# Kernel optimization log

Hardware: AMD Instinct MI355X
Metric: run time of the kernel (lower is better)

The kernel has to match this reference:

```python
import jax, jax.numpy as jnp
import numpy as np

B, N, D = 32, 2048, 16
PCD = 2        # point_cloud_dimensions
K_NN = 16      # k nearest neighbours
FILTERS = 64


def setup_inputs() -> dict:
    key = jax.random.key(0)
    k1, k2, k3 = jax.random.split(key, 3)
    x = jax.random.normal(k1, (B, N, D), dtype=jnp.float32)
    # 1x1 Conv2D == dense over the last (channel) dim: W [D, FILTERS], b [FILTERS]
    W = jax.random.normal(k2, (D, FILTERS), dtype=jnp.float32) * (1.0 / np.sqrt(D))
    b = jnp.zeros((FILTERS,), dtype=jnp.float32)
    return {"x": x, "W": W, "b": b}


def reference(x, W, b):
    # points = first PCD channels; features = full input (dynamic_coordinates=True)
    points = x[:, :, :PCD]                                   # [B,N,PCD]
    # squared pairwise distances: ||p_i||^2 + ||p_j||^2 - 2 p_i.p_j  -> [B,N,N]
    sq = jnp.sum(points * points, axis=-1)                   # [B,N]
    dist = sq[:, :, None] + sq[:, None, :] - 2.0 * jnp.einsum(
        'bnd,bmd->bnm', points, points)
    # k nearest neighbours (smallest distance) per point -> [B,N,k]
    _, idx = jax.lax.top_k(-dist, K_NN)
    # gather neighbour features: [B,N,k,D]
    neigh = jax.vmap(lambda f, i: f[i])(x, idx)
    centre = x[:, :, None, :]                                # [B,N,1,D]
    # NOTE: source concatenates along the neighbour axis -> [B,N,k+1,D]
    edges = jnp.concatenate([centre, neigh - centre], axis=2)
    # 1x1 conv (linear activation) over channel dim: [B,N,k+1,FILTERS]
    conv = jnp.einsum('bnkd,df->bnkf', edges, W) + b
    # Max pooling over neighbour axis: [B,N,FILTERS]
    pooled = jnp.max(conv, axis=2)
    # shortcut_input_features=True: concat original features
    return jnp.concatenate([pooled, x], axis=-1)             # [B,N,FILTERS+D]
```

## Files before the change

### kernel.cpp

```cpp
#include <hip/hip_runtime.h>


#define B_  32
#define N_  2048
#define D_  16
#define F_  64
#define K_  16
#define OUTD (F_ + D_)
#define NQ  64
#define NS  4
#define SPLIT (N_ / NS)

__global__ __launch_bounds__(256) void proj_kernel(const float* __restrict__ x,
                                                   const float* __restrict__ W,
                                                   float* __restrict__ Y) {
    __shared__ float Ws[D_ * F_];
    __shared__ float xs[4][D_];
    const int t = threadIdx.x;
    for (int i = t; i < D_ * F_; i += 256) Ws[i] = W[i];
    const int p0 = blockIdx.x * 4;
    if (t < 4 * D_) {
        int pw = t / D_, d = t % D_;
        xs[pw][d] = x[(size_t)(p0 + pw) * D_ + d];
    }
    __syncthreads();
    const int w = t >> 6, f = t & 63;
    float acc = 0.f;
#pragma unroll
    for (int d = 0; d < D_; d++) acc = fmaf(xs[w][d], Ws[d * F_ + f], acc);
    Y[(size_t)(p0 + w) * F_ + f] = acc;
}

__global__ __launch_bounds__(256) void knn_kernel(const float* __restrict__ x,
                                                  int* __restrict__ idx) {
    __shared__ float2 pts[N_];
    __shared__ float  sqs[N_];
    __shared__ float  arr[NS - 1][NQ * 17];
    __shared__ float  Tq[NQ];
    __shared__ int    cnt[NQ];
    __shared__ unsigned short tiebuf[NS][NQ][K_];
    __shared__ int    tiecnt[NS][NQ];

    const int b = blockIdx.x >> 5;
    const int qbase = (blockIdx.x & 31) * NQ;
    const int t = threadIdx.x;
    const int s = t >> 6;
    const int qi = t & 63;
    const int q = qbase + qi;

    const float* xb = x + (size_t)b * N_ * D_;
    for (int m = t; m < N_; m += 256) {
        float2 p = make_float2(xb[m * D_ + 0], xb[m * D_ + 1]);
        pts[m] = p;
        sqs[m] = __fadd_rn(__fmul_rn(p.x, p.x), __fmul_rn(p.y, p.y));
    }
    if (t < NQ) cnt[t] = 0;
    __syncthreads();

    const float2 qp = pts[q];
    const float sqn = sqs[q];

    float key[K_];
#pragma unroll
    for (int j = 0; j < K_; j++) key[j] = INFINITY;

    const int m0 = s * SPLIT, m1 = m0 + SPLIT;
#pragma unroll 2
    for (int m = m0; m < m1; m += 2) {
        float2 pa = pts[m];     float sa = sqs[m];
        float2 pb = pts[m + 1]; float sb = sqs[m + 1];
        float dota = __fmaf_rn(qp.y, pa.y, __fmul_rn(qp.x, pa.x));
        float da   = __fsub_rn(__fadd_rn(sqn, sa), __fmul_rn(2.f, dota));
        float dotb = __fmaf_rn(qp.y, pb.y, __fmul_rn(qp.x, pb.x));
        float db   = __fsub_rn(__fadd_rn(sqn, sb), __fmul_rn(2.f, dotb));
        float y0 = fminf(da, db), y1 = fmaxf(da, db);
#pragma unroll
        for (int j = K_ - 1; j >= 2; j--)
            key[j] = fminf(fminf(key[j], fmaxf(key[j - 1], y0)),
                           fmaxf(key[j - 2], y1));
        key[1] = fminf(fminf(key[1], fmaxf(key[0], y0)), y1);
        key[0] = fminf(key[0], y0);
    }

    if (s > 0) {
#pragma unroll
        for (int j = 0; j < K_; j++) arr[s - 1][qi * 17 + j] = key[j];
    }
    __syncthreads();

    if (s == 0) {
        for (int ss = 0; ss < NS - 1; ss++) {
#pragma unroll
            for (int j = 0; j < K_; j += 2) {
                float y0 = arr[ss][qi * 17 + j];
                float y1 = arr[ss][qi * 17 + j + 1];
#pragma unroll
                for (int jj = K_ - 1; jj >= 2; jj--)
                    key[jj] = fminf(fminf(key[jj], fmaxf(key[jj - 1], y0)),
                                    fmaxf(key[jj - 2], y1));
                key[1] = fminf(fminf(key[1], fmaxf(key[0], y0)), y1);
                key[0] = fminf(key[0], y0);
            }
        }
        Tq[qi] = key[K_ - 1];
    }
    __syncthreads();

    const float T = Tq[qi];
    int* op = idx + ((size_t)b * N_ + q) * K_;
    int tc = 0;
    for (int m = m0; m < m1; m++) {
        float2 p = pts[m];
        float dot = __fmaf_rn(qp.y, p.y, __fmul_rn(qp.x, p.x));
        float d   = __fsub_rn(__fadd_rn(sqn, sqs[m]), __fmul_rn(2.f, dot));
        if (d < T) {
            int slot = atomicAdd(&cnt[qi], 1);
            op[slot] = m;
        } else if (d == T) {
            if (tc < K_) tiebuf[s][qi][tc] = (unsigned short)m;
            tc++;
        }
    }
    tiecnt[s][qi] = (tc < K_) ? tc : K_;
    __syncthreads();

    if (s == 0) {
        int c1 = cnt[qi];
        int w = c1;
        int need = K_ - c1;
        for (int ss = 0; ss < NS && need > 0; ss++) {
            int nn = tiecnt[ss][qi];
            for (int j = 0; j < nn && need > 0; j++) {
                op[w++] = (int)tiebuf[ss][qi][j];
                need--;
            }
        }
    }
}

__global__ __launch_bounds__(256) void pool_kernel(const float* __restrict__ x,
                                                   const float* __restrict__ bias,
                                                   const float* __restrict__ Y,
                                                   const int* __restrict__ idx,
                                                   float* __restrict__ out) {
    const int t = threadIdx.x;
    const int w = t >> 6, f = t & 63;
    const int p = blockIdx.x * 4 + w;
    const int b = p >> 11;
    const size_t pb = (size_t)p;

    const float yn = Y[pb * F_ + f];
    const int* ip = idx + pb * K_;
    float M = -INFINITY;
#pragma unroll
    for (int k = 0; k < K_; k++) {
        int m = ip[k];
        float ym = Y[((size_t)b * N_ + m) * F_ + f];
        M = fmaxf(M, ym);
    }
    float pooled = fmaxf(yn, M - yn) + bias[f];
    out[pb * OUTD + f] = pooled;
    if (f < D_) out[pb * OUTD + F_ + f] = x[pb * D_ + f];
}

extern "C" void kernel_launch(void* const* d_in, const int* in_sizes, int n_in,
                              void* d_out, int out_size, void* d_ws, size_t ws_size,
                              hipStream_t stream) {
    const float* x    = (const float*)d_in[0];
    const float* W    = (const float*)d_in[1];
    const float* bias = (const float*)d_in[2];
    float* out = (float*)d_out;

    float* Y  = (float*)d_ws;
    int*  idx = (int*)((char*)d_ws + (size_t)B_ * N_ * F_ * 4);

    proj_kernel<<<B_ * N_ / 4, 256, 0, stream>>>(x, W, Y);
    knn_kernel <<<B_ * (N_ / NQ), 256, 0, stream>>>(x, idx);
    pool_kernel<<<B_ * N_ / 4, 256, 0, stream>>>(x, bias, Y, idx, out);
}
```

Before: 293.8 us.

## Process more points per block and alias kNN tie buffer onto merge scratch

The projection and pooling kernels now handle 16 points per block (4 per wavefront) rather than 4. This amortises the weight-tile load into shared memory and the bias load, and cuts the block count by a factor of four. The kNN kernel reuses the cross-split merge array as its tie buffer to shrink its shared-memory footprint, and declares a minimum of 4 blocks per multiprocessor so more blocks can be resident. The aliasing relies on the merge array being fully consumed before tie writes begin, which the existing barrier ensures. The occupancy hint may force register limits on the sorting network.

New measurement: 290.0 us. About the same (-1.3%).

```diff
diff --git a/kernel.cpp b/kernel.cpp
--- a/kernel.cpp
+++ b/kernel.cpp
@@ -15,31 +15,33 @@
                                                    const float* __restrict__ W,
                                                    float* __restrict__ Y) {
     __shared__ float Ws[D_ * F_];
-    __shared__ float xs[4][D_];
+    __shared__ float xs[16][D_];
     const int t = threadIdx.x;
     for (int i = t; i < D_ * F_; i += 256) Ws[i] = W[i];
-    const int p0 = blockIdx.x * 4;
-    if (t < 4 * D_) {
-        int pw = t / D_, d = t % D_;
-        xs[pw][d] = x[(size_t)(p0 + pw) * D_ + d];
-    }
+    const int p0 = blockIdx.x * 16;
+    ((float*)xs)[t] = x[(size_t)p0 * D_ + t];
     __syncthreads();
     const int w = t >> 6, f = t & 63;
-    float acc = 0.f;
 #pragma unroll
-    for (int d = 0; d < D_; d++) acc = fmaf(xs[w][d], Ws[d * F_ + f], acc);
-    Y[(size_t)(p0 + w) * F_ + f] = acc;
+    for (int i = 0; i < 4; i++) {
+        const int pw = w * 4 + i;
+        float acc = 0.f;
+#pragma unroll
+        for (int d = 0; d < D_; d++) acc = fmaf(xs[pw][d], Ws[d * F_ + f], acc);
+        Y[(size_t)(p0 + pw) * F_ + f] = acc;
+    }
 }
 
-__global__ __launch_bounds__(256) void knn_kernel(const float* __restrict__ x,
-                                                  int* __restrict__ idx) {
+__global__ __launch_bounds__(256, 4) void knn_kernel(const float* __restrict__ x,
+                                                     int* __restrict__ idx) {
     __shared__ float2 pts[N_];
     __shared__ float  sqs[N_];
-    __shared__ float  arr[NS - 1][NQ * 17];
+    __shared__ float  arr_raw[NS - 1][NQ * 17];
     __shared__ float  Tq[NQ];
     __shared__ int    cnt[NQ];
-    __shared__ unsigned short tiebuf[NS][NQ][K_];
     __shared__ int    tiecnt[NS][NQ];
+    unsigned short (*tiebuf)[NQ][K_] =
+        (unsigned short (*)[NQ][K_])&arr_raw[0][0];
 
     const int b = blockIdx.x >> 5;
     const int qbase = (blockIdx.x & 31) * NQ;
@@ -84,7 +86,7 @@
 
     if (s > 0) {
 #pragma unroll
-        for (int j = 0; j < K_; j++) arr[s - 1][qi * 17 + j] = key[j];
+        for (int j = 0; j < K_; j++) arr_raw[s - 1][qi * 17 + j] = key[j];
     }
     __syncthreads();
 
@@ -92,8 +94,8 @@
         for (int ss = 0; ss < NS - 1; ss++) {
 #pragma unroll
             for (int j = 0; j < K_; j += 2) {
-                float y0 = arr[ss][qi * 17 + j];
-                float y1 = arr[ss][qi * 17 + j + 1];
+                float y0 = arr_raw[ss][qi * 17 + j];
+                float y1 = arr_raw[ss][qi * 17 + j + 1];
 #pragma unroll
                 for (int jj = K_ - 1; jj >= 2; jj--)
                     key[jj] = fminf(fminf(key[jj], fmaxf(key[jj - 1], y0)),
@@ -145,22 +147,26 @@
                                                    float* __restrict__ out) {
     const int t = threadIdx.x;
     const int w = t >> 6, f = t & 63;
-    const int p = blockIdx.x * 4 + w;
-    const int b = p >> 11;
-    const size_t pb = (size_t)p;
+    const float bf = bias[f];
+#pragma unroll
+    for (int i = 0; i < 4; i++) {
+        const int p = blockIdx.x * 16 + w * 4 + i;
+        const int b = p >> 11;
+        const size_t pb = (size_t)p;
 
-    const float yn = Y[pb * F_ + f];
-    const int* ip = idx + pb * K_;
-    float M = -INFINITY;
+        const float yn = Y[pb * F_ + f];
+        const int* ip = idx + pb * K_;
+        float M = -INFINITY;
 #pragma unroll
-    for (int k = 0; k < K_; k++) {
-        int m = ip[k];
-        float ym = Y[((size_t)b * N_ + m) * F_ + f];
-        M = fmaxf(M, ym);
+        for (int k = 0; k < K_; k++) {
+            int m = ip[k];
+            float ym = Y[((size_t)b * N_ + m) * F_ + f];
+            M = fmaxf(M, ym);
+        }
+        float pooled = fmaxf(yn, M - yn) + bf;
+        out[pb * OUTD + f] = pooled;
+        if (f < D_) out[pb * OUTD + F_ + f] = x[pb * D_ + f];
     }
-    float pooled = fmaxf(yn, M - yn) + bias[f];
-    out[pb * OUTD + f] = pooled;
-    if (f < D_) out[pb * OUTD + F_ + f] = x[pb * D_ + f];
 }
 
 extern "C" void kernel_launch(void* const* d_in, const int* in_sizes, int n_in,
@@ -174,7 +180,7 @@
     float* Y  = (float*)d_ws;
     int*  idx = (int*)((char*)d_ws + (size_t)B_ * N_ * F_ * 4);
 
-    proj_kernel<<<B_ * N_ / 4, 256, 0, stream>>>(x, W, Y);
+    proj_kernel<<<B_ * N_ / 16, 256, 0, stream>>>(x, W, Y);
     knn_kernel <<<B_ * (N_ / NQ), 256, 0, stream>>>(x, idx);
-    pool_kernel<<<B_ * N_ / 4, 256, 0, stream>>>(x, bias, Y, idx, out);
+    pool_kernel<<<B_ * N_ / 16, 256, 0, stream>>>(x, bias, Y, idx, out);
 }
```
